# Optimization experiments

Hardware: AMD Instinct MI355X
Metric: run time of the kernel (lower is better)

The kernel has to match this reference:

```python
import jax, jax.numpy as jnp
import numpy as np

C = 0.11512925464970229  # ln(10)/20
K = 15
FD = 128
FS = 160
OV = 40
MAX_LAG = 256
PAD_L = K // 2
PAD_R = K - 1 - PAD_L
LOG_GAIN_LIMIT = 10 * C
GAIN_A = (6.0 * C - (-6.0 * C)) / 2
GAIN_B = (6.0 * C + (-6.0 * C)) / 2


def setup_inputs() -> dict:
    key = jax.random.key(0)
    ks = jax.random.split(key, 8)
    B, NF = 32, 500
    N = NF * FS
    x = jax.random.normal(ks[0], (B, 1, N), dtype=jnp.float32)
    features = jax.random.normal(ks[1], (B, NF, FD), dtype=jnp.float32)
    lags = jax.random.randint(ks[2], (B, NF), 0, 256)
    s = 1.0 / np.sqrt(FD)
    ck_w = jax.random.normal(ks[3], (K, FD), dtype=jnp.float32) * s
    ck_b = jax.random.normal(ks[4], (K,), dtype=jnp.float32) * 0.01
    fg_w = jax.random.normal(ks[5], (1, FD), dtype=jnp.float32) * s
    fg_b = jnp.full((1,), max(0.1, 4.0 + LOG_GAIN_LIMIT), dtype=jnp.float32)
    gg_w = jax.random.normal(ks[6], (1, FD), dtype=jnp.float32) * s
    gg_b = jax.random.normal(ks[7], (1,), dtype=jnp.float32) * 0.01
    return {"x": x, "features": features, "lags": lags,
            "ck_w": ck_w, "ck_b": ck_b, "fg_w": fg_w, "fg_b": fg_b,
            "gg_w": gg_w, "gg_b": gg_b}


def reference(x, features, lags, ck_w, ck_b, fg_w, fg_b, gg_w, gg_b):
    B, _, N = x.shape
    NF = features.shape[1]
    OUT = FS + OV  # per-frame output length before crossfade

    # per-frame FIR kernels, p=2 normalized over taps
    kernels = jnp.einsum('bfd,kd->bfk', features, ck_w) + ck_b          # (B,NF,K)
    kernels = kernels / (1e-6 + jnp.sqrt(jnp.sum(kernels**2, -1, keepdims=True)))
    # per-frame scalar gains
    gains = jnp.exp(-jax.nn.relu(features @ fg_w[0] + fg_b[0]) + LOG_GAIN_LIMIT)   # (B,NF)
    ggains = jnp.exp(GAIN_A * jnp.tanh(features @ gg_w[0] + gg_b[0]) + GAIN_B)     # (B,NF)

    # pad: [PAD_L,PAD_R] for conv, then [MAX_LAG, OV] for lag gather / final frame
    xp = jnp.pad(x[:, 0, :], ((0, 0), (MAX_LAG + PAD_L, PAD_R + OV)))   # (B,Np)

    L = FS + K - 1 + OV
    t = jnp.arange(L)
    f_off = jnp.arange(NF) * FS
    cidx = t[None, None, :] + f_off[None, :, None] + MAX_LAG - lags[:, :, None]  # (B,NF,L)
    xx = xp[jnp.arange(B)[:, None, None], cidx]                         # (B,NF,L)

    # grouped conv1d == cross-correlation with per-frame kernel
    win = jnp.stack([xx[:, :, k:k + OUT] for k in range(K)], axis=-1)   # (B,NF,OUT,K)
    conv = jnp.einsum('bflk,bfk->bfl', win, kernels)                    # (B,NF,OUT)

    # dry path
    offset = MAX_LAG + PAD_L
    pt_idx = offset + f_off[:, None] + jnp.arange(OUT)[None, :]         # (NF,OUT)
    pt = xp[:, pt_idx]                                                  # (B,NF,OUT)

    new_chunk = ggains[:, :, None] * (conv * gains[:, :, None] + pt)    # (B,NF,OUT)

    # overlap-add crossfade between consecutive frames
    win2 = 0.5 + 0.5 * jnp.cos((jnp.arange(OV) + 0.5) * jnp.pi / OV)
    win1 = win2[::-1]
    tails = new_chunk[:, :, FS:]                                        # (B,NF,OV)
    prev = jnp.concatenate([jnp.zeros_like(tails[:, :1]), tails[:, :-1]], axis=1)
    head = new_chunk[:, :, :OV] * win1 + prev * win2
    out = jnp.concatenate([head, new_chunk[:, :, OV:FS]], axis=-1)      # (B,NF,FS)
    return out.reshape(B, 1, NF * FS)
```

## Files before the change

kernel.cpp:

```cpp
#include <hip/hip_runtime.h>
#include <math.h>

namespace {
constexpr int K = 15;
constexpr int FD = 128;
constexpr int FS = 160;
constexpr int OV = 40;
constexpr int NFRAMES = 500;
constexpr int NSAMP = NFRAMES * FS;
constexpr float C_CONST = 0.11512925464970229f;
constexpr float LOG_GAIN_LIMIT = 10.0f * C_CONST;
constexpr float GAIN_A = 6.0f * C_CONST;
constexpr float PI_F = 3.14159265358979323846f;

constexpr int K1FPB = 15;
constexpr int SFSTR = 132;

constexpr int FPB = 10;
constexpr int NFR = FPB + 1;
constexpr int NW4 = 55;
constexpr int WINA = 220;
}

__global__ __launch_bounds__(256)
void params_kernel(const float* __restrict__ feat,
                   const float* __restrict__ ck_w,
                   const float* __restrict__ ck_b,
                   const float* __restrict__ fg_w,
                   const float* __restrict__ fg_b,
                   const float* __restrict__ gg_w,
                   const float* __restrict__ gg_b,
                   float* __restrict__ params,
                   int G)
{
    const int tid = threadIdx.x;
    const int g0  = blockIdx.x * K1FPB;

    __shared__ __align__(16) float sfeat[K1FPB][SFSTR];
    __shared__ float sdots[K1FPB][17];

    for (int i = tid; i < K1FPB * (FD / 4); i += 256) {
        const int fi = i >> 5;
        const int e4 = i & 31;
        const int g  = g0 + fi;
        float4 v = make_float4(0.f, 0.f, 0.f, 0.f);
        if (g < G) v = ((const float4*)feat)[(size_t)g * (FD / 4) + e4];
        *(float4*)&sfeat[fi][e4 * 4] = v;
    }
    __syncthreads();

    if (tid < K1FPB * 17) {
        const int fi = tid / 17;
        const int j  = tid - fi * 17;
        const float* wrow = (j < K) ? (ck_w + (size_t)j * FD)
                                    : ((j == K) ? fg_w : gg_w);
        const float4* w4 = (const float4*)wrow;
        const float4* f4 = (const float4*)&sfeat[fi][0];
        float4 acc = make_float4(0.f, 0.f, 0.f, 0.f);
        #pragma unroll
        for (int i = 0; i < FD / 4; ++i) {
            const float4 a = f4[i];
            const float4 w = w4[i];
            acc.x += a.x * w.x; acc.y += a.y * w.y;
            acc.z += a.z * w.z; acc.w += a.w * w.w;
        }
        const float bias = (j < K) ? ck_b[j] : ((j == K) ? fg_b[0] : gg_b[0]);
        sdots[fi][j] = acc.x + acc.y + acc.z + acc.w + bias;
    }
    __syncthreads();

    if (tid < K1FPB) {
        const int g = g0 + tid;
        if (g < G) {
            float kern[K];
            float n2 = 0.f;
            #pragma unroll
            for (int k = 0; k < K; ++k) {
                kern[k] = sdots[tid][k];
                n2 += kern[k] * kern[k];
            }
            const float inv   = 1.f / (1e-6f + sqrtf(n2));
            const float gain  = expf(-fmaxf(sdots[tid][K], 0.f) + LOG_GAIN_LIMIT);
            const float ggain = expf(GAIN_A * tanhf(sdots[tid][K + 1]));
            const float ks    = ggain * gain * inv;
            float p[16];
            #pragma unroll
            for (int k = 0; k < K; ++k) p[k] = ks * kern[k];
            p[15] = ggain;
            float4* dst = (float4*)(params + (size_t)g * 16);
            dst[0] = *(float4*)&p[0];
            dst[1] = *(float4*)&p[4];
            dst[2] = *(float4*)&p[8];
            dst[3] = *(float4*)&p[12];
        }
    }
}

__global__ __launch_bounds__(256)
void synth_kernel(const float* __restrict__ x,
                  const int*   __restrict__ lags,
                  const float* __restrict__ params,
                  float* __restrict__ out)
{
    const int tid = threadIdx.x;
    const int bid = blockIdx.x;
    const int b   = bid / (NFRAMES / FPB);
    const int blk = bid - b * (NFRAMES / FPB);
    const int f0  = blk * FPB;

    __shared__ __align__(16) float swin[NFR][WINA];
    __shared__ __align__(16) float sfk[NFR][16];
    __shared__ __align__(16) float swin2[OV + 8];

    const float* xb = x + (size_t)b * NSAMP;

    for (int i = tid; i < NFR * NW4; i += 256) {
        const int fr = i / NW4;
        const int m  = i - fr * NW4;
        const int pf = f0 - 1 + fr;
        float4 v = make_float4(0.f, 0.f, 0.f, 0.f);
        if (pf >= 0) {
            const int base = pf * FS - lags[b * NFRAMES + pf] - 7;
            const int idx  = base + 4 * m;
            if (idx >= 0 && idx + 3 < NSAMP) {
                v = *(const float4*)(xb + idx);
            } else {
                if (idx     >= 0 && idx     < NSAMP) v.x = xb[idx];
                if (idx + 1 >= 0 && idx + 1 < NSAMP) v.y = xb[idx + 1];
                if (idx + 2 >= 0 && idx + 2 < NSAMP) v.z = xb[idx + 2];
                if (idx + 3 >= 0 && idx + 3 < NSAMP) v.w = xb[idx + 3];
            }
        }
        *(float4*)&swin[fr][4 * m] = v;
    }

    if (tid < NFR * 4) {
        const int fr = tid >> 2;
        const int q  = tid & 3;
        const int pf = f0 - 1 + fr;
        float4 v = make_float4(0.f, 0.f, 0.f, 0.f);
        if (pf >= 0)
            v = ((const float4*)(params + ((size_t)b * NFRAMES + pf) * 16))[q];
        *(float4*)&sfk[fr][q * 4] = v;
    }

    if (tid >= 64 && tid < 64 + OV) {
        const int t = tid - 64;
        swin2[t] = 0.5f + 0.5f * cosf(((float)t + 0.5f) * (PI_F / OV));
    }
    __syncthreads();

    const int obase = f0 * FS;
    for (int g = tid; g < FPB * (FS / 4); g += 256) {
        const int frl = g / (FS / 4);
        const int gi  = g - frl * (FS / 4);
        const int t   = gi * 4;
        const int fr  = frl + 1;

        const float4 k0 = *(const float4*)&sfk[fr][0];
        const float4 k1 = *(const float4*)&sfk[fr][4];
        const float4 k2 = *(const float4*)&sfk[fr][8];
        const float4 k3 = *(const float4*)&sfk[fr][12];
        const float kc[16] = {k0.x,k0.y,k0.z,k0.w, k1.x,k1.y,k1.z,k1.w,
                              k2.x,k2.y,k2.z,k2.w, k3.x,k3.y,k3.z,k3.w};

        float w[20];
        #pragma unroll
        for (int q = 0; q < 5; ++q)
            *(float4*)&w[4 * q] = *(const float4*)&swin[fr][t + 4 * q];

        const float4 pt = *(const float4*)(xb + obase + frl * FS + t);

        float4 res;
        {
            float c0 = 0.f, c1 = 0.f, c2 = 0.f, c3 = 0.f;
            #pragma unroll
            for (int k = 0; k < K; ++k) {
                const float kk = kc[k];
                c0 += w[k]     * kk;
                c1 += w[k + 1] * kk;
                c2 += w[k + 2] * kk;
                c3 += w[k + 3] * kk;
            }
            const float ps = kc[15];
            res.x = c0 + ps * pt.x; res.y = c1 + ps * pt.y;
            res.z = c2 + ps * pt.z; res.w = c3 + ps * pt.w;
        }

        if (gi < OV / 4) {
            const float4 q0 = *(const float4*)&sfk[fr - 1][0];
            const float4 q1 = *(const float4*)&sfk[fr - 1][4];
            const float4 q2 = *(const float4*)&sfk[fr - 1][8];
            const float4 q3 = *(const float4*)&sfk[fr - 1][12];
            const float qc[16] = {q0.x,q0.y,q0.z,q0.w, q1.x,q1.y,q1.z,q1.w,
                                  q2.x,q2.y,q2.z,q2.w, q3.x,q3.y,q3.z,q3.w};
            float wv[20];
            #pragma unroll
            for (int q = 0; q < 5; ++q)
                *(float4*)&wv[4 * q] = *(const float4*)&swin[fr - 1][FS + t + 4 * q];

            float c0 = 0.f, c1 = 0.f, c2 = 0.f, c3 = 0.f;
            #pragma unroll
            for (int k = 0; k < K; ++k) {
                const float kk = qc[k];
                c0 += wv[k]     * kk;
                c1 += wv[k + 1] * kk;
                c2 += wv[k + 2] * kk;
                c3 += wv[k + 3] * kk;
            }
            const float ps = qc[15];
            const float4 tail = make_float4(c0 + ps * pt.x, c1 + ps * pt.y,
                                            c2 + ps * pt.z, c3 + ps * pt.w);
            const float4 w2 = *(const float4*)&swin2[t];
            res.x = res.x * (1.f - w2.x) + tail.x * w2.x;
            res.y = res.y * (1.f - w2.y) + tail.y * w2.y;
            res.z = res.z * (1.f - w2.z) + tail.z * w2.z;
            res.w = res.w * (1.f - w2.w) + tail.w * w2.w;
        }

        *(float4*)(out + (size_t)b * NSAMP + obase + frl * FS + t) = res;
    }
}

extern "C" void kernel_launch(void* const* d_in, const int* in_sizes, int n_in,
                              void* d_out, int out_size, void* d_ws, size_t ws_size,
                              hipStream_t stream) {
    const float* x    = (const float*)d_in[0];
    const float* feat = (const float*)d_in[1];
    const int*   lags = (const int*)d_in[2];
    const float* ck_w = (const float*)d_in[3];
    const float* ck_b = (const float*)d_in[4];
    const float* fg_w = (const float*)d_in[5];
    const float* fg_b = (const float*)d_in[6];
    const float* gg_w = (const float*)d_in[7];
    const float* gg_b = (const float*)d_in[8];
    float* out    = (float*)d_out;
    float* params = (float*)d_ws;

    const int B = in_sizes[0] / NSAMP;
    const int G = B * NFRAMES;

    const int nblk1 = (G + K1FPB - 1) / K1FPB;
    params_kernel<<<dim3(nblk1), dim3(256), 0, stream>>>(
        feat, ck_w, ck_b, fg_w, fg_b, gg_w, gg_b, params, G);

    const int nblk2 = B * (NFRAMES / FPB);
    synth_kernel<<<dim3(nblk2), dim3(256), 0, stream>>>(
        x, lags, params, out);
}
```

Before: 110.1 us.

## Drop shared-memory staging in synth kernel; load windows directly per thread

The synth kernel now maps one thread to each group of four output samples across the whole batch and reads its lagged input window and per-frame parameters straight from global memory. This replaces per-block shared staging of 10-frame windows, __syncthreads and the leftover idle threads in the last loop pass. It also computes the crossfade window inline with cosf. The cost is overlapping, often unaligned (lag-dependent) global reads that go through cache instead of being shared, plus redundant cos and parameter loads per thread.

```diff
diff --git a/kernel.cpp b/kernel.cpp
--- a/kernel.cpp
+++ b/kernel.cpp
@@ -15,11 +15,7 @@
 
 constexpr int K1FPB = 15;
 constexpr int SFSTR = 132;
-
-constexpr int FPB = 10;
-constexpr int NFR = FPB + 1;
-constexpr int NW4 = 55;
-constexpr int WINA = 220;
+constexpr int GPF = FS / 4;
 }
 
 __global__ __launch_bounds__(256)
@@ -100,104 +96,84 @@
 void synth_kernel(const float* __restrict__ x,
                   const int*   __restrict__ lags,
                   const float* __restrict__ params,
-                  float* __restrict__ out)
+                  float* __restrict__ out,
+                  int total)
 {
-    const int tid = threadIdx.x;
-    const int bid = blockIdx.x;
-    const int b   = bid / (NFRAMES / FPB);
-    const int blk = bid - b * (NFRAMES / FPB);
-    const int f0  = blk * FPB;
-
-    __shared__ __align__(16) float swin[NFR][WINA];
-    __shared__ __align__(16) float sfk[NFR][16];
-    __shared__ __align__(16) float swin2[OV + 8];
+    const int gidx = blockIdx.x * 256 + threadIdx.x;
+    if (gidx >= total) return;
+    const int b  = gidx / (NFRAMES * GPF);
+    const int r  = gidx - b * (NFRAMES * GPF);
+    const int f  = r / GPF;
+    const int gi = r - f * GPF;
+    const int t  = gi * 4;
 
     const float* xb = x + (size_t)b * NSAMP;
 
-    for (int i = tid; i < NFR * NW4; i += 256) {
-        const int fr = i / NW4;
-        const int m  = i - fr * NW4;
-        const int pf = f0 - 1 + fr;
-        float4 v = make_float4(0.f, 0.f, 0.f, 0.f);
-        if (pf >= 0) {
-            const int base = pf * FS - lags[b * NFRAMES + pf] - 7;
-            const int idx  = base + 4 * m;
-            if (idx >= 0 && idx + 3 < NSAMP) {
-                v = *(const float4*)(xb + idx);
+    float w[20];
+    {
+        const int base = f * FS - lags[b * NFRAMES + f] - 7 + t;
+        if (base >= 0 && base + 19 < NSAMP) {
+            #pragma unroll
+            for (int q = 0; q < 5; ++q)
+                *(float4*)&w[4 * q] = *(const float4*)(xb + base + 4 * q);
+        } else {
+            #pragma unroll
+            for (int j = 0; j < 20; ++j) {
+                const int idx = base + j;
+                w[j] = (idx >= 0 && idx < NSAMP) ? xb[idx] : 0.f;
+            }
+        }
+    }
+
+    float kc[16];
+    {
+        const float4* pp = (const float4*)(params + ((size_t)b * NFRAMES + f) * 16);
+        #pragma unroll
+        for (int q = 0; q < 4; ++q) *(float4*)&kc[4 * q] = pp[q];
+    }
+
+    const float4 pt = *(const float4*)(xb + f * FS + t);
+
+    float4 res;
+    {
+        float c0 = 0.f, c1 = 0.f, c2 = 0.f, c3 = 0.f;
+        #pragma unroll
+        for (int k = 0; k < K; ++k) {
+            const float kk = kc[k];
+            c0 += w[k]     * kk;
+            c1 += w[k + 1] * kk;
+            c2 += w[k + 2] * kk;
+            c3 += w[k + 3] * kk;
+        }
+        const float ps = kc[15];
+        res.x = c0 + ps * pt.x; res.y = c1 + ps * pt.y;
+        res.z = c2 + ps * pt.z; res.w = c3 + ps * pt.w;
+    }
+
+    if (gi < OV / 4) {
+        float4 w2;
+        w2.x = 0.5f + 0.5f * cosf(((float)t + 0.5f) * (PI_F / OV));
+        w2.y = 0.5f + 0.5f * cosf(((float)t + 1.5f) * (PI_F / OV));
+        w2.z = 0.5f + 0.5f * cosf(((float)t + 2.5f) * (PI_F / OV));
+        w2.w = 0.5f + 0.5f * cosf(((float)t + 3.5f) * (PI_F / OV));
+        if (f > 0) {
+            float wv[20];
+            const int base2 = (f - 1) * FS - lags[b * NFRAMES + f - 1] - 7 + FS + t;
+            if (base2 >= 0 && base2 + 19 < NSAMP) {
+                #pragma unroll
+                for (int q = 0; q < 5; ++q)
+                    *(float4*)&wv[4 * q] = *(const float4*)(xb + base2 + 4 * q);
             } else {
-                if (idx     >= 0 && idx     < NSAMP) v.x = xb[idx];
-                if (idx + 1 >= 0 && idx + 1 < NSAMP) v.y = xb[idx + 1];
-                if (idx + 2 >= 0 && idx + 2 < NSAMP) v.z = xb[idx + 2];
-                if (idx + 3 >= 0 && idx + 3 < NSAMP) v.w = xb[idx + 3];
-            }
-        }
-        *(float4*)&swin[fr][4 * m] = v;
-    }
-
-    if (tid < NFR * 4) {
-        const int fr = tid >> 2;
-        const int q  = tid & 3;
-        const int pf = f0 - 1 + fr;
-        float4 v = make_float4(0.f, 0.f, 0.f, 0.f);
-        if (pf >= 0)
-            v = ((const float4*)(params + ((size_t)b * NFRAMES + pf) * 16))[q];
-        *(float4*)&sfk[fr][q * 4] = v;
-    }
-
-    if (tid >= 64 && tid < 64 + OV) {
-        const int t = tid - 64;
-        swin2[t] = 0.5f + 0.5f * cosf(((float)t + 0.5f) * (PI_F / OV));
-    }
-    __syncthreads();
-
-    const int obase = f0 * FS;
-    for (int g = tid; g < FPB * (FS / 4); g += 256) {
-        const int frl = g / (FS / 4);
-        const int gi  = g - frl * (FS / 4);
-        const int t   = gi * 4;
-        const int fr  = frl + 1;
-
-        const float4 k0 = *(const float4*)&sfk[fr][0];
-        const float4 k1 = *(const float4*)&sfk[fr][4];
-        const float4 k2 = *(const float4*)&sfk[fr][8];
-        const float4 k3 = *(const float4*)&sfk[fr][12];
-        const float kc[16] = {k0.x,k0.y,k0.z,k0.w, k1.x,k1.y,k1.z,k1.w,
-                              k2.x,k2.y,k2.z,k2.w, k3.x,k3.y,k3.z,k3.w};
-
-        float w[20];
-        #pragma unroll
-        for (int q = 0; q < 5; ++q)
-            *(float4*)&w[4 * q] = *(const float4*)&swin[fr][t + 4 * q];
-
-        const float4 pt = *(const float4*)(xb + obase + frl * FS + t);
-
-        float4 res;
-        {
-            float c0 = 0.f, c1 = 0.f, c2 = 0.f, c3 = 0.f;
-            #pragma unroll
-            for (int k = 0; k < K; ++k) {
-                const float kk = kc[k];
-                c0 += w[k]     * kk;
-                c1 += w[k + 1] * kk;
-                c2 += w[k + 2] * kk;
-                c3 += w[k + 3] * kk;
-            }
-            const float ps = kc[15];
-            res.x = c0 + ps * pt.x; res.y = c1 + ps * pt.y;
-            res.z = c2 + ps * pt.z; res.w = c3 + ps * pt.w;
-        }
-
-        if (gi < OV / 4) {
-            const float4 q0 = *(const float4*)&sfk[fr - 1][0];
-            const float4 q1 = *(const float4*)&sfk[fr - 1][4];
-            const float4 q2 = *(const float4*)&sfk[fr - 1][8];
-            const float4 q3 = *(const float4*)&sfk[fr - 1][12];
-            const float qc[16] = {q0.x,q0.y,q0.z,q0.w, q1.x,q1.y,q1.z,q1.w,
-                                  q2.x,q2.y,q2.z,q2.w, q3.x,q3.y,q3.z,q3.w};
-            float wv[20];
-            #pragma unroll
-            for (int q = 0; q < 5; ++q)
-                *(float4*)&wv[4 * q] = *(const float4*)&swin[fr - 1][FS + t + 4 * q];
+                #pragma unroll
+                for (int j = 0; j < 20; ++j) {
+                    const int idx = base2 + j;
+                    wv[j] = (idx >= 0 && idx < NSAMP) ? xb[idx] : 0.f;
+                }
+            }
+            float qc[16];
+            const float4* qq = (const float4*)(params + ((size_t)b * NFRAMES + f - 1) * 16);
+            #pragma unroll
+            for (int q = 0; q < 4; ++q) *(float4*)&qc[4 * q] = qq[q];
 
             float c0 = 0.f, c1 = 0.f, c2 = 0.f, c3 = 0.f;
             #pragma unroll
@@ -211,15 +187,17 @@
             const float ps = qc[15];
             const float4 tail = make_float4(c0 + ps * pt.x, c1 + ps * pt.y,
                                             c2 + ps * pt.z, c3 + ps * pt.w);
-            const float4 w2 = *(const float4*)&swin2[t];
             res.x = res.x * (1.f - w2.x) + tail.x * w2.x;
             res.y = res.y * (1.f - w2.y) + tail.y * w2.y;
             res.z = res.z * (1.f - w2.z) + tail.z * w2.z;
             res.w = res.w * (1.f - w2.w) + tail.w * w2.w;
-        }
-
-        *(float4*)(out + (size_t)b * NSAMP + obase + frl * FS + t) = res;
-    }
+        } else {
+            res.x *= (1.f - w2.x); res.y *= (1.f - w2.y);
+            res.z *= (1.f - w2.z); res.w *= (1.f - w2.w);
+        }
+    }
+
+    *(float4*)(out + (size_t)b * NSAMP + f * FS + t) = res;
 }
 
 extern "C" void kernel_launch(void* const* d_in, const int* in_sizes, int n_in,
@@ -244,7 +222,8 @@
     params_kernel<<<dim3(nblk1), dim3(256), 0, stream>>>(
         feat, ck_w, ck_b, fg_w, fg_b, gg_w, gg_b, params, G);
 
-    const int nblk2 = B * (NFRAMES / FPB);
+    const int total = G * GPF;
+    const int nblk2 = (total + 255) / 256;
     synth_kernel<<<dim3(nblk2), dim3(256), 0, stream>>>(
-        x, lags, params, out);
-}
+        x, lags, params, out, total);
+}
```

After: 111.0 us. Within noise of the previous version (+0.8%).
